# Optimization experiments

Hardware: AMD Instinct MI355X
Metric: run time of the kernel (lower is better)

Reference implementation:

```python
import jax, jax.numpy as jnp
import numpy as np

THRESHOLD = 0.15  # init kwarg


def setup_inputs() -> dict:
    key = jax.random.key(0)
    B, T, N = 64, 1024, 512
    inputs = jax.random.normal(key, (B, T, N), dtype=jnp.float32)
    return {"inputs": inputs}


def reference(inputs) -> jnp.ndarray:
    # inputs: [B, T, N]; Pearson correlation across the sample (time) axis.
    B, T, N = inputs.shape
    xc = inputs - jnp.mean(inputs, axis=1, keepdims=True)        # [B,T,N]
    cov = jnp.einsum('bti,btj->bij', xc, xc)                     # [B,N,N] (unnormalized; norm cancels)
    d = jnp.sqrt(jnp.diagonal(cov, axis1=1, axis2=2))            # [B,N]
    corr = cov / (d[:, :, None] * d[:, None, :])                 # [B,N,N]

    # Original loop: for i<j, if |corr[:,i,j]|>thr: mask = mask * one_hot(i).
    # Equivalent closed form: let fired[b,i] = any_{j>i} |corr[b,i,j]|>thr.
    #   0 fired rows -> all-ones mask
    #   1 fired row  -> one_hot of that i (repeated onehot(i) multiplies are idempotent)
    #   >=2 distinct fired rows -> onehot(i1)*onehot(i2)=0 -> all-zeros mask
    upper = jnp.triu(jnp.ones((N, N), dtype=bool), k=1)
    cond = (jnp.abs(corr) > THRESHOLD) & upper                   # [B,N,N]
    fired = jnp.any(cond, axis=2)                                # [B,N]
    num_fired = jnp.sum(fired, axis=1)                           # [B]

    ones = jnp.ones((B, N), dtype=jnp.float32)
    mask = jnp.where((num_fired == 0)[:, None], ones,
                     jnp.where((num_fired == 1)[:, None],
                               fired.astype(jnp.float32),
                               jnp.zeros_like(ones)))
    return mask
```

## Files before the change

kernel.cpp:

```cpp
#include <hip/hip_runtime.h>
#include <hip/hip_bf16.h>

#define BB 64
#define TT 1024
#define NN 512
#define LISTCAP (1u << 18)

static constexpr float THR = 0.15f;

typedef __attribute__((ext_vector_type(8))) short bf16x8;
typedef __attribute__((ext_vector_type(4))) float f32x4;

__device__ __forceinline__ void gload16(const void* g, void* lds_dst) {
    __builtin_amdgcn_global_load_lds(
        (const __attribute__((address_space(1))) unsigned int*)g,
        (__attribute__((address_space(3))) unsigned int*)lds_dst, 16, 0, 0);
}

__global__ __launch_bounds__(512) void transpose_colsum(
    const float* __restrict__ x, ushort* __restrict__ xbf,
    float* __restrict__ s1, float* __restrict__ dv,
    float* __restrict__ nv, float* __restrict__ nl,
    unsigned* __restrict__ fired, unsigned* __restrict__ cnt) {
    __shared__ float red[3][8][64];
    int b = blockIdx.x, ng = blockIdx.y;
    int n0 = ng * 64;
    int tid = threadIdx.x, w = tid >> 6, l = tid & 63;
    const float* xb = x + (size_t)b * TT * NN + n0 + l;
    float a1 = 0.f, a2 = 0.f, al = 0.f;
    if (b == 0 && ng == 0 && tid == 64) *cnt = 0;

    char* xbase = (char*)xbf + ((size_t)(b * 8 + ng) * 32) * 4096
                  + (unsigned)l * 64u
                  + (((unsigned)(w & 3) ^ (((unsigned)l >> 1) & 3u)) << 4);

    for (int tc = 0; tc < 2; ++tc) {
        #pragma unroll
        for (int i = 0; i < 8; ++i) {
            int t0 = tc * 512 + i * 64 + w * 8;
            unsigned hp[4];
            #pragma unroll
            for (int q = 0; q < 4; ++q) {
                float v0 = xb[(size_t)(t0 + 2 * q) * NN];
                float v1 = xb[(size_t)(t0 + 2 * q + 1) * NN];
                a1 += v0 + v1;
                a2 += v0 * v0 + v1 * v1;
                unsigned u0 = __float_as_uint(v0), u1 = __float_as_uint(v1);
                float h0 = __uint_as_float(u0 & 0xFFFF0000u);
                float h1 = __uint_as_float(u1 & 0xFFFF0000u);
                float l0 = v0 - h0, l1 = v1 - h1;
                al += l0 * l0 + l1 * l1;
                hp[q] = (u0 >> 16) | (u1 & 0xFFFF0000u);
            }
            *(uint4*)(xbase + (size_t)(t0 >> 5) * 4096) =
                make_uint4(hp[0], hp[1], hp[2], hp[3]);
        }
    }
    red[0][w][l] = a1; red[1][w][l] = a2; red[2][w][l] = al;
    __syncthreads();
    if (tid < 64) {
        float r1 = 0.f, r2 = 0.f, rl = 0.f;
        #pragma unroll
        for (int k = 0; k < 8; ++k) {
            r1 += red[0][k][tid]; r2 += red[1][k][tid]; rl += red[2][k][tid];
        }
        size_t o = (size_t)b * NN + n0 + tid;
        s1[o] = r1;
        dv[o] = r2 - r1 * r1 * (1.0f / TT);
        nv[o] = sqrtf(r2);
        nl[o] = sqrtf(rl);
        fired[o] = 0u;
    }
}

__global__ __launch_bounds__(256, 8) void corr_mfma(
    const ushort* __restrict__ xbf, const float* __restrict__ s1,
    const float* __restrict__ dv, const float* __restrict__ nv,
    const float* __restrict__ nl, unsigned* __restrict__ fired,
    unsigned* __restrict__ cnt, unsigned* __restrict__ list) {
    __shared__ uint4 ldsbuf[1024];
    char* base = (char*)ldsbuf;

    int id = blockIdx.x;
    int swz = ((id & 7) * 288) + (id >> 3);
    int b = swz / 36;
    int u = swz % 36;
    int ti = 0, rem = u;
    while (rem >= (8 - ti)) { rem -= (8 - ti); ++ti; }
    int tj = ti + rem;
    int i0 = ti * 64, j0 = tj * 64;
    bool diag = (ti == tj);

    int tid = threadIdx.x;
    int wave = tid >> 6, lane = tid & 63;
    int rl = lane & 15, kg = lane >> 4;

    const char* srcA = (const char*)xbf + ((size_t)(b * 8 + ti) * 32) * 4096 + tid * 16;
    const char* srcB = (const char*)xbf + ((size_t)(b * 8 + tj) * 32) * 4096 + tid * 16;

    auto STAGE = [&](int s, int buf) {
        char* d = base + (buf << 13) + wave * 1024;
        gload16(srcA + (size_t)s * 4096, d);
        if (!diag) gload16(srcB + (size_t)s * 4096, d + 4096);
    };

    int wr = wave >> 1, wc = wave & 1;
    bool skip_mm = diag && (wr == 1) && (wc == 0);

    unsigned aoff[2], boff[2];
    #pragma unroll
    for (int f = 0; f < 2; ++f) {
        unsigned ca = (unsigned)(32 * wr + 16 * f + rl);
        aoff[f] = ca * 64u + ((((unsigned)kg ^ ((ca >> 1) & 3u)) & 3u) << 4);
        unsigned cb2 = (unsigned)(32 * wc + 16 * f + rl);
        boff[f] = cb2 * 64u + ((((unsigned)kg ^ ((cb2 >> 1) & 3u)) & 3u) << 4);
    }
    unsigned bbase = diag ? 0u : 4096u;

    f32x4 acc[2][2];
    #pragma unroll
    for (int i = 0; i < 2; ++i)
        #pragma unroll
        for (int j = 0; j < 2; ++j)
            acc[i][j] = (f32x4)0.0f;

    STAGE(0, 0);
    __syncthreads();

    for (int it = 0; it < 32; ++it) {
        if (it + 1 < 32) STAGE(it + 1, (it + 1) & 1);

        const char* cb = base + ((it & 1) << 13);
        if (!skip_mm) {
            bf16x8 A[2], Bv[2];
            #pragma unroll
            for (int f = 0; f < 2; ++f) A[f] = *(const bf16x8*)(cb + aoff[f]);
            #pragma unroll
            for (int f = 0; f < 2; ++f) Bv[f] = *(const bf16x8*)(cb + bbase + boff[f]);
            #pragma unroll
            for (int fj = 0; fj < 2; ++fj)
                #pragma unroll
                for (int fi = 0; fi < 2; ++fi)
                    acc[fi][fj] = __builtin_amdgcn_mfma_f32_16x16x32_bf16(
                        A[fi], Bv[fj], acc[fi][fj], 0, 0, 0);
        }
        __syncthreads();
    }

    const float thr2 = THR * THR;
    const float invT = 1.0f / TT;
    const float* s1b = s1 + (size_t)b * NN;
    const float* dvb = dv + (size_t)b * NN;
    const float* nvb = nv + (size_t)b * NN;
    const float* nlb = nl + (size_t)b * NN;
    unsigned* fb = fired + (size_t)b * NN;
    int rowb = i0 + 32 * wr + kg * 4;
    int colb = j0 + 32 * wc + rl;
    #pragma unroll
    for (int fj = 0; fj < 2; ++fj) {
        int gj = colb + 16 * fj;
        float sj = s1b[gj], djv = dvb[gj];
        float nvj = nvb[gj], nlj = nlb[gj];
        #pragma unroll
        for (int fi = 0; fi < 2; ++fi) {
            int gi0 = rowb + 16 * fi;
            #pragma unroll
            for (int r = 0; r < 4; ++r) {
                int gi = gi0 + r;
                if (gj > gi) {
                    float cc = acc[fi][fj][r] - s1b[gi] * sj * invT;
                    float lim = thr2 * dvb[gi] * djv;
                    float nvi = nvb[gi], nli = nlb[gi];
                    float B = nli * nvj + nlj * nvi + 3.0f * nli * nlj
                              + 1e-3f * nvi * nvj;
                    float a = fabsf(cc);
                    float lo = a - B;
                    if (lo > 0.0f && lo * lo > lim) {
                        atomicOr(&fb[gi], 1u);
                    } else if ((a + B) * (a + B) > lim) {
                        unsigned idx = atomicAdd(cnt, 1u);
                        if (idx < LISTCAP)
                            list[idx] = ((unsigned)b << 18) | ((unsigned)gi << 9)
                                        | (unsigned)gj;
                    }
                }
            }
        }
    }
}

__global__ __launch_bounds__(256) void cleanup_pairs(
    const float* __restrict__ x, const float* __restrict__ s1,
    const float* __restrict__ dv, const unsigned* __restrict__ cnt,
    const unsigned* __restrict__ list, unsigned* __restrict__ fired) {
    unsigned n = *cnt;
    if (n > LISTCAP) n = LISTCAP;
    int lane = threadIdx.x & 63;
    int gw = (blockIdx.x * 256 + threadIdx.x) >> 6;
    int nw = (gridDim.x * 256) >> 6;
    for (unsigned p = gw; p < n; p += nw) {
        unsigned e = list[p];
        int b = e >> 18, i = (e >> 9) & 511, j = e & 511;
        const float* xb = x + (size_t)b * TT * NN;
        double s = 0.0;
        for (int t = lane; t < TT; t += 64)
            s += (double)xb[(size_t)t * NN + i] * (double)xb[(size_t)t * NN + j];
        #pragma unroll
        for (int o = 32; o > 0; o >>= 1)
            s += __shfl_xor(s, o, 64);
        if (lane == 0) {
            double cov = s - (double)s1[(size_t)b * NN + i]
                             * (double)s1[(size_t)b * NN + j] / (double)TT;
            double lim = (double)THR * (double)THR
                         * (double)dv[(size_t)b * NN + i]
                         * (double)dv[(size_t)b * NN + j];
            if (cov * cov > lim) atomicOr(&fired[(size_t)b * NN + i], 1u);
        }
    }
}

__global__ __launch_bounds__(512) void finalize_mask(
    const unsigned* __restrict__ fired, float* __restrict__ out) {
    int b = blockIdx.x;
    int n = threadIdx.x;
    unsigned f = fired[(size_t)b * NN + n];
    __shared__ int wsum[8];
    unsigned long long m = __ballot(f != 0u);
    int lane = n & 63;
    int w = n >> 6;
    if (lane == 0) wsum[w] = __popcll(m);
    __syncthreads();
    int cnt = 0;
    #pragma unroll
    for (int i = 0; i < 8; ++i) cnt += wsum[i];
    float val = (cnt == 0) ? 1.0f : ((cnt == 1) ? (f ? 1.0f : 0.0f) : 0.0f);
    out[(size_t)b * NN + n] = val;
}

extern "C" void kernel_launch(void* const* d_in, const int* in_sizes, int n_in,
                              void* d_out, int out_size, void* d_ws, size_t ws_size,
                              hipStream_t stream) {
    const float* x = (const float*)d_in[0];
    float* out = (float*)d_out;

    ushort* xbf = (ushort*)d_ws;
    float* s1 = (float*)(xbf + (size_t)BB * NN * TT);
    float* dv = s1 + (size_t)BB * NN;
    float* nv = dv + (size_t)BB * NN;
    float* nl = nv + (size_t)BB * NN;
    unsigned* fired = (unsigned*)(nl + (size_t)BB * NN);
    unsigned* cnt   = fired + (size_t)BB * NN;
    unsigned* list  = cnt + 16;

    transpose_colsum<<<dim3(BB, 8), 512, 0, stream>>>(x, xbf, s1, dv, nv, nl,
                                                      fired, cnt);
    corr_mfma<<<dim3(2304), 256, 0, stream>>>(xbf, s1, dv, nv, nl, fired, cnt, list);
    cleanup_pairs<<<128, 256, 0, stream>>>(x, s1, dv, cnt, list, fired);
    finalize_mask<<<BB, 512, 0, stream>>>(fired, out);
}
```

Measured before the change: 87.36 us.

## Quantize inputs to int8 and use i8 MFMA for covariance screening

```diff
diff --git a/kernel.cpp b/kernel.cpp
--- a/kernel.cpp
+++ b/kernel.cpp
@@ -7,9 +7,10 @@
 #define LISTCAP (1u << 18)
 
 static constexpr float THR = 0.15f;
-
-typedef __attribute__((ext_vector_type(8))) short bf16x8;
-typedef __attribute__((ext_vector_type(4))) float f32x4;
+static constexpr float SQ    = 6.0f / 127.0f;
+static constexpr float INVSQ = 127.0f / 6.0f;
+
+typedef __attribute__((ext_vector_type(4))) int i32x4;
 
 __device__ __forceinline__ void gload16(const void* g, void* lds_dst) {
     __builtin_amdgcn_global_load_lds(
@@ -18,64 +19,67 @@
 }
 
 __global__ __launch_bounds__(512) void transpose_colsum(
-    const float* __restrict__ x, ushort* __restrict__ xbf,
+    const float* __restrict__ x, char* __restrict__ xq,
     float* __restrict__ s1, float* __restrict__ dv,
-    float* __restrict__ nv, float* __restrict__ nl,
+    float* __restrict__ nh, float* __restrict__ nl,
     unsigned* __restrict__ fired, unsigned* __restrict__ cnt) {
-    __shared__ float red[3][8][64];
+    __shared__ float red[4][8][64];
     int b = blockIdx.x, ng = blockIdx.y;
     int n0 = ng * 64;
     int tid = threadIdx.x, w = tid >> 6, l = tid & 63;
     const float* xb = x + (size_t)b * TT * NN + n0 + l;
     float a1 = 0.f, a2 = 0.f, al = 0.f;
+    int aq = 0;
     if (b == 0 && ng == 0 && tid == 64) *cnt = 0;
 
-    char* xbase = (char*)xbf + ((size_t)(b * 8 + ng) * 32) * 4096
+    char* pbase = xq + ((size_t)(b * 8 + ng) * 16) * 4096
                   + (unsigned)l * 64u
-                  + (((unsigned)(w & 3) ^ (((unsigned)l >> 1) & 3u)) << 4);
+                  + ((((unsigned)(w >> 1)) ^ (((unsigned)l >> 1) & 3u)) << 4)
+                  + (unsigned)(w & 1) * 8u;
 
     for (int tc = 0; tc < 2; ++tc) {
         #pragma unroll
         for (int i = 0; i < 8; ++i) {
             int t0 = tc * 512 + i * 64 + w * 8;
-            unsigned hp[4];
-            #pragma unroll
-            for (int q = 0; q < 4; ++q) {
-                float v0 = xb[(size_t)(t0 + 2 * q) * NN];
-                float v1 = xb[(size_t)(t0 + 2 * q + 1) * NN];
-                a1 += v0 + v1;
-                a2 += v0 * v0 + v1 * v1;
-                unsigned u0 = __float_as_uint(v0), u1 = __float_as_uint(v1);
-                float h0 = __uint_as_float(u0 & 0xFFFF0000u);
-                float h1 = __uint_as_float(u1 & 0xFFFF0000u);
-                float l0 = v0 - h0, l1 = v1 - h1;
-                al += l0 * l0 + l1 * l1;
-                hp[q] = (u0 >> 16) | (u1 & 0xFFFF0000u);
+            unsigned lo = 0, hi = 0;
+            #pragma unroll
+            for (int j = 0; j < 8; ++j) {
+                float v = xb[(size_t)(t0 + j) * NN];
+                a1 += v;
+                a2 += v * v;
+                int q = __float2int_rn(v * INVSQ);
+                q = q > 127 ? 127 : (q < -127 ? -127 : q);
+                aq += q * q;
+                float lr = fmaf((float)q, -SQ, v);
+                al += lr * lr;
+                unsigned byte = (unsigned)(q & 255);
+                if (j < 4) lo |= byte << (8 * j);
+                else       hi |= byte << (8 * (j - 4));
             }
-            *(uint4*)(xbase + (size_t)(t0 >> 5) * 4096) =
-                make_uint4(hp[0], hp[1], hp[2], hp[3]);
-        }
-    }
-    red[0][w][l] = a1; red[1][w][l] = a2; red[2][w][l] = al;
+            *(uint2*)(pbase + (size_t)(t0 >> 6) * 4096) = make_uint2(lo, hi);
+        }
+    }
+    red[0][w][l] = a1; red[1][w][l] = a2; red[2][w][l] = (float)aq; red[3][w][l] = al;
     __syncthreads();
     if (tid < 64) {
-        float r1 = 0.f, r2 = 0.f, rl = 0.f;
+        float r1 = 0.f, r2 = 0.f, rq = 0.f, rl = 0.f;
         #pragma unroll
         for (int k = 0; k < 8; ++k) {
-            r1 += red[0][k][tid]; r2 += red[1][k][tid]; rl += red[2][k][tid];
+            r1 += red[0][k][tid]; r2 += red[1][k][tid];
+            rq += red[2][k][tid]; rl += red[3][k][tid];
         }
         size_t o = (size_t)b * NN + n0 + tid;
         s1[o] = r1;
         dv[o] = r2 - r1 * r1 * (1.0f / TT);
-        nv[o] = sqrtf(r2);
+        nh[o] = SQ * sqrtf(rq);
         nl[o] = sqrtf(rl);
         fired[o] = 0u;
     }
 }
 
 __global__ __launch_bounds__(256, 8) void corr_mfma(
-    const ushort* __restrict__ xbf, const float* __restrict__ s1,
-    const float* __restrict__ dv, const float* __restrict__ nv,
+    const char* __restrict__ xq, const float* __restrict__ s1,
+    const float* __restrict__ dv, const float* __restrict__ nh,
     const float* __restrict__ nl, unsigned* __restrict__ fired,
     unsigned* __restrict__ cnt, unsigned* __restrict__ list) {
     __shared__ uint4 ldsbuf[1024];
@@ -95,8 +99,8 @@
     int wave = tid >> 6, lane = tid & 63;
     int rl = lane & 15, kg = lane >> 4;
 
-    const char* srcA = (const char*)xbf + ((size_t)(b * 8 + ti) * 32) * 4096 + tid * 16;
-    const char* srcB = (const char*)xbf + ((size_t)(b * 8 + tj) * 32) * 4096 + tid * 16;
+    const char* srcA = xq + ((size_t)(b * 8 + ti) * 16) * 4096 + tid * 16;
+    const char* srcB = xq + ((size_t)(b * 8 + tj) * 16) * 4096 + tid * 16;
 
     auto STAGE = [&](int s, int buf) {
         char* d = base + (buf << 13) + wave * 1024;
@@ -117,31 +121,30 @@
     }
     unsigned bbase = diag ? 0u : 4096u;
 
-    f32x4 acc[2][2];
+    i32x4 acc[2][2];
     #pragma unroll
     for (int i = 0; i < 2; ++i)
         #pragma unroll
         for (int j = 0; j < 2; ++j)
-            acc[i][j] = (f32x4)0.0f;
+            acc[i][j] = (i32x4)0;
 
     STAGE(0, 0);
     __syncthreads();
 
-    for (int it = 0; it < 32; ++it) {
-        if (it + 1 < 32) STAGE(it + 1, (it + 1) & 1);
-
+    for (int it = 0; it < 16; ++it) {
+        if (it + 1 < 16) STAGE(it + 1, (it + 1) & 1);
         const char* cb = base + ((it & 1) << 13);
         if (!skip_mm) {
-            bf16x8 A[2], Bv[2];
-            #pragma unroll
-            for (int f = 0; f < 2; ++f) A[f] = *(const bf16x8*)(cb + aoff[f]);
-            #pragma unroll
-            for (int f = 0; f < 2; ++f) Bv[f] = *(const bf16x8*)(cb + bbase + boff[f]);
+            i32x4 A[2], Bv[2];
+            #pragma unroll
+            for (int f = 0; f < 2; ++f) A[f] = *(const i32x4*)(cb + aoff[f]);
+            #pragma unroll
+            for (int f = 0; f < 2; ++f) Bv[f] = *(const i32x4*)(cb + bbase + boff[f]);
             #pragma unroll
             for (int fj = 0; fj < 2; ++fj)
                 #pragma unroll
                 for (int fi = 0; fi < 2; ++fi)
-                    acc[fi][fj] = __builtin_amdgcn_mfma_f32_16x16x32_bf16(
+                    acc[fi][fj] = __builtin_amdgcn_mfma_i32_16x16x64_i8(
                         A[fi], Bv[fj], acc[fi][fj], 0, 0, 0);
         }
         __syncthreads();
@@ -149,9 +152,10 @@
 
     const float thr2 = THR * THR;
     const float invT = 1.0f / TT;
+    const float s2 = SQ * SQ;
     const float* s1b = s1 + (size_t)b * NN;
     const float* dvb = dv + (size_t)b * NN;
-    const float* nvb = nv + (size_t)b * NN;
+    const float* nhb = nh + (size_t)b * NN;
     const float* nlb = nl + (size_t)b * NN;
     unsigned* fb = fired + (size_t)b * NN;
     int rowb = i0 + 32 * wr + kg * 4;
@@ -160,7 +164,7 @@
     for (int fj = 0; fj < 2; ++fj) {
         int gj = colb + 16 * fj;
         float sj = s1b[gj], djv = dvb[gj];
-        float nvj = nvb[gj], nlj = nlb[gj];
+        float nhj = nhb[gj], nlj = nlb[gj];
         #pragma unroll
         for (int fi = 0; fi < 2; ++fi) {
             int gi0 = rowb + 16 * fi;
@@ -168,11 +172,11 @@
             for (int r = 0; r < 4; ++r) {
                 int gi = gi0 + r;
                 if (gj > gi) {
-                    float cc = acc[fi][fj][r] - s1b[gi] * sj * invT;
+                    float cc = s2 * (float)acc[fi][fj][r] - s1b[gi] * sj * invT;
                     float lim = thr2 * dvb[gi] * djv;
-                    float nvi = nvb[gi], nli = nlb[gi];
-                    float B = nli * nvj + nlj * nvi + 3.0f * nli * nlj
-                              + 1e-3f * nvi * nvj;
+                    float nhi = nhb[gi], nli = nlb[gi];
+                    float B = nli * nhj + nlj * nhi + nli * nlj
+                              + 1e-3f * nhi * nhj;
                     float a = fabsf(cc);
                     float lo = a - B;
                     if (lo > 0.0f && lo * lo > lim) {
@@ -243,18 +247,18 @@
     const float* x = (const float*)d_in[0];
     float* out = (float*)d_out;
 
-    ushort* xbf = (ushort*)d_ws;
-    float* s1 = (float*)(xbf + (size_t)BB * NN * TT);
+    char* xq = (char*)d_ws;
+    float* s1 = (float*)(xq + (size_t)BB * NN * TT);
     float* dv = s1 + (size_t)BB * NN;
-    float* nv = dv + (size_t)BB * NN;
-    float* nl = nv + (size_t)BB * NN;
+    float* nh = dv + (size_t)BB * NN;
+    float* nl = nh + (size_t)BB * NN;
     unsigned* fired = (unsigned*)(nl + (size_t)BB * NN);
     unsigned* cnt   = fired + (size_t)BB * NN;
     unsigned* list  = cnt + 16;
 
-    transpose_colsum<<<dim3(BB, 8), 512, 0, stream>>>(x, xbf, s1, dv, nv, nl,
+    transpose_colsum<<<dim3(BB, 8), 512, 0, stream>>>(x, xq, s1, dv, nh, nl,
                                                       fired, cnt);
-    corr_mfma<<<dim3(2304), 256, 0, stream>>>(xbf, s1, dv, nv, nl, fired, cnt, list);
+    corr_mfma<<<dim3(2304), 256, 0, stream>>>(xq, s1, dv, nh, nl, fired, cnt, list);
     cleanup_pairs<<<128, 256, 0, stream>>>(x, s1, dv, cnt, list, fired);
     finalize_mask<<<BB, 512, 0, stream>>>(fired, out);
 }
```

Measured after the change: 103.9 us. 1.19x slower.
